# Kernel tuning notes

Hardware: AMD Instinct MI355X
Metric: run time of the kernel (lower is better)

The kernel has to match this reference:

```python
import jax, jax.numpy as jnp
import numpy as np

B, H, S, D = 2, 16, 2048, 64  # batch, heads, seq (q_len=k_len), head dim (d_k=d_v)


def setup_inputs() -> dict:
    key = jax.random.key(0)
    kq, kk, kv = jax.random.split(key, 3)
    Q = jax.random.normal(kq, (B, H, S, D), dtype=jnp.float32)
    K = jax.random.normal(kk, (B, H, S, D), dtype=jnp.float32)
    V = jax.random.normal(kv, (B, H, S, D), dtype=jnp.float32)
    # causal 0/1 mask [q_len, k_len]; zeros get filled with -inf like masked_fill_
    mask = jnp.tril(jnp.ones((S, S), dtype=jnp.int32))
    return {"Q": Q, "K": K, "V": V, "mask": mask}


def reference(Q, K, V, mask):
    scale = K.shape[-1] ** 0.5
    # [B,H,q,k] = Q @ K^T / sqrt(d_k)
    scores = jnp.einsum("bhqd,bhkd->bhqk", Q, K) / scale
    # mask broadcast over batch/heads; mask==0 -> -inf
    scores = jnp.where(mask == 0, jnp.float32(-jnp.inf), scores)
    attn = jax.nn.softmax(scores, axis=-1)
    return jnp.einsum("bhqk,bhkd->bhqd", attn, V)
```

## Files before the change

kernel.cpp:

```cpp
#include <hip/hip_runtime.h>

#define S_LEN 2048
#define DHEAD 64
#define BK 64
#define NBH 32
#define QSCALE 0.18033688011112042f
#define LTHR 1.125899907e15f
#define LSCL 8.881784197e-16f

typedef float f32x4 __attribute__((ext_vector_type(4)));
typedef __bf16 bf16x8 __attribute__((ext_vector_type(8)));
typedef unsigned short u16x8 __attribute__((ext_vector_type(8)));
typedef unsigned short u16x4 __attribute__((ext_vector_type(4)));
typedef unsigned int   u32x4 __attribute__((ext_vector_type(4)));
typedef unsigned int   u32x2 __attribute__((ext_vector_type(2)));

static __device__ __forceinline__ unsigned short bfr(float f) {
    return __builtin_bit_cast(unsigned short, (__bf16)f);
}
static __device__ __forceinline__ int swz(int row, int cb) {
    return row * 128 + (cb ^ ((row & 7) << 4));
}

#if __has_builtin(__builtin_amdgcn_permlane32_swap) && __has_builtin(__builtin_amdgcn_permlane16_swap)
static __device__ __forceinline__ void plswap32(unsigned& a, unsigned& b) {
    u32x2 r = __builtin_amdgcn_permlane32_swap(a, b, false, false);
    a = r[0]; b = r[1];
}
static __device__ __forceinline__ void plswap16(unsigned& a, unsigned& b) {
    u32x2 r = __builtin_amdgcn_permlane16_swap(a, b, false, false);
    a = r[0]; b = r[1];
}
#else
static __device__ __forceinline__ void plswap32(unsigned& a, unsigned& b) {
    asm("v_permlane32_swap_b32 %0, %1" : "+v"(a), "+v"(b));
}
static __device__ __forceinline__ void plswap16(unsigned& a, unsigned& b) {
    asm("v_permlane16_swap_b32 %0, %1" : "+v"(a), "+v"(b));
}
#endif

__global__ __launch_bounds__(256)
void prep(const float* __restrict__ K, const float* __restrict__ V,
          unsigned short* __restrict__ Kb, unsigned short* __restrict__ Vt, int n4) {
    __shared__ unsigned short t2[64][72];
    if ((int)blockIdx.x < 2048) {
        const int stride = 2048 * 256;
        for (int i = (int)blockIdx.x * 256 + threadIdx.x; i < n4; i += stride) {
            f32x4 v = ((const f32x4*)K)[i];
            u16x4 t;
            t[0] = bfr(v[0]); t[1] = bfr(v[1]); t[2] = bfr(v[2]); t[3] = bfr(v[3]);
            ((u16x4*)Kb)[i] = t;
        }
    } else {
        const int bid = (int)blockIdx.x - 2048;
        const int bh = bid >> 5;
        const int st = bid & 31;
        const int t  = threadIdx.x;
        {
            const int sl = t >> 2, d0 = (t & 3) * 16;
            const float* src = V + ((size_t)bh * S_LEN + st * 64 + sl) * DHEAD + d0;
#pragma unroll
            for (int j = 0; j < 4; ++j) {
                f32x4 v = *(const f32x4*)(src + j * 4);
#pragma unroll
                for (int e = 0; e < 4; ++e) t2[sl][d0 + j * 4 + e] = bfr(v[e]);
            }
        }
        __syncthreads();
        const int d = t >> 2, sc = (t & 3) * 16;
        u16x8 a, b;
#pragma unroll
        for (int r = 0; r < 8; ++r) { a[r] = t2[sc + r][d]; b[r] = t2[sc + 8 + r][d]; }
        unsigned short* dst = Vt + ((size_t)bh * DHEAD + d) * S_LEN + st * 64 + sc;
        *(u16x8*)dst = a;
        *(u16x8*)(dst + 8) = b;
    }
}

__global__ __launch_bounds__(256, 3)
void attn_pipe(const float* __restrict__ Qg,
               const unsigned short* __restrict__ Kb,
               const unsigned short* __restrict__ Vt,
               float* __restrict__ Og) {
    __shared__ __align__(16) unsigned short sK[2][BK * DHEAD];
    __shared__ __align__(16) unsigned short sV[2][DHEAD * BK];

    const int tid  = threadIdx.x;
    const int lane = tid & 63;
    const int w    = tid >> 6;
    const int idx = (int)blockIdx.x >> 5;
    const int bh  = (int)blockIdx.x & (NBH - 1);
    const int jj  = idx & 7, k4 = idx >> 3;
    const int blk_q = (k4 == 0) ? 31 - jj : (k4 == 1) ? jj
                    : (k4 == 2) ? 16 + jj : 15 - jj;
    const int q0 = blk_q * 64;
    const size_t base = (size_t)bh * (S_LEN * DHEAD);

    const int c = lane & 15;
    const int h = lane >> 4;

    const int srow = w * 8 + (lane >> 3);
    const int ch8  = ((lane & 7) ^ (lane >> 3)) * 8;
    const unsigned short* pK = Kb + base + (size_t)srow * DHEAD + ch8;
    const unsigned short* pV = Vt + base + (size_t)srow * S_LEN + ch8;

    auto issue = [&](int buf, int kt) {
        unsigned short* dK = &sK[buf][w * 512];
        unsigned short* dV = &sV[buf][w * 512];
        const unsigned short* gk = pK + (size_t)kt * 4096;
        const unsigned short* gv = pV + kt * 64;
#pragma unroll
        for (int i = 0; i < 2; ++i) {
            __builtin_amdgcn_global_load_lds(
                (const __attribute__((address_space(1))) unsigned int*)(gk + i * 2048),
                (__attribute__((address_space(3))) unsigned int*)(dK + i * 2048),
                16, 0, 0);
            __builtin_amdgcn_global_load_lds(
                (const __attribute__((address_space(1))) unsigned int*)(gv + (size_t)i * 32 * S_LEN),
                (__attribute__((address_space(3))) unsigned int*)(dV + i * 2048),
                16, 0, 0);
        }
    };

    bf16x8 qf[2];
    {
        const int qrow = q0 + w * 16 + c;
        const float* qp = Qg + base + (size_t)qrow * DHEAD + h * 8;
#pragma unroll
        for (int kk = 0; kk < 2; ++kk) {
            f32x4 a = *(const f32x4*)(qp + kk * 32);
            f32x4 b = *(const f32x4*)(qp + kk * 32 + 4);
            u16x8 t;
#pragma unroll
            for (int j = 0; j < 4; ++j) {
                t[j]     = bfr(a[j] * QSCALE);
                t[4 + j] = bfr(b[j] * QSCALE);
            }
            qf[kk] = __builtin_bit_cast(bf16x8, t);
        }
    }

    bf16x8 onesf;
    {
        u16x8 t;
#pragma unroll
        for (int j = 0; j < 8; ++j) t[j] = 0x3F80;
        onesf = __builtin_bit_cast(bf16x8, t);
    }

    int offAB[4][2];
#pragma unroll
    for (int n = 0; n < 4; ++n)
#pragma unroll
        for (int kk = 0; kk < 2; ++kk)
            offAB[n][kk] = swz(n * 16 + c, (kk * 32 + h * 8) * 2);

    f32x4 o[4];
#pragma unroll
    for (int dn = 0; dn < 4; ++dn) o[dn] = (f32x4){0.f, 0.f, 0.f, 0.f};
    f32x4 l4 = (f32x4){0.f, 0.f, 0.f, 0.f};
    float m_run = 0.f;
    const int qg = q0 + w * 16 + c;

    issue(0, 0);
    __syncthreads();
    if (blk_q >= 1) issue(1, 1);

    f32x4 st[4];
    {
        const char* sKc = (const char*)&sK[0][0];
#pragma unroll
        for (int n = 0; n < 4; ++n) {
            f32x4 acc = (f32x4){0.f, 0.f, 0.f, 0.f};
#pragma unroll
            for (int kk = 0; kk < 2; ++kk) {
                u16x8 kf = *(const u16x8*)(sKc + offAB[n][kk]);
                acc = __builtin_amdgcn_mfma_f32_16x16x32_bf16(
                        __builtin_bit_cast(bf16x8, kf), qf[kk], acc, 0, 0, 0);
            }
            st[n] = acc;
        }
    }
    bf16x8 vf[4][2];
    {
        const char* sVc = (const char*)&sV[0][0];
#pragma unroll
        for (int dn = 0; dn < 4; ++dn)
#pragma unroll
            for (int kk = 0; kk < 2; ++kk)
                vf[dn][kk] = __builtin_bit_cast(bf16x8,
                                *(const u16x8*)(sVc + offAB[dn][kk]));
    }

    for (int i = 0; i <= blk_q; ++i) {
        f32x4 st2[4];
        bf16x8 vf2[4][2];
        if (i < blk_q) {
            __syncthreads();
            if (i + 2 <= blk_q) issue(i & 1, i + 2);

            const char* sKc = (const char*)&sK[(i + 1) & 1][0];
            const char* sVc = (const char*)&sV[(i + 1) & 1][0];
            const float mb = -m_run;
#pragma unroll
            for (int n = 0; n < 4; ++n) {
                f32x4 acc = (f32x4){mb, mb, mb, mb};
#pragma unroll
                for (int kk = 0; kk < 2; ++kk) {
                    u16x8 kf = *(const u16x8*)(sKc + offAB[n][kk]);
                    acc = __builtin_amdgcn_mfma_f32_16x16x32_bf16(
                            __builtin_bit_cast(bf16x8, kf), qf[kk], acc, 0, 0, 0);
                }
                st2[n] = acc;
            }
#pragma unroll
            for (int dn = 0; dn < 4; ++dn)
#pragma unroll
                for (int kk = 0; kk < 2; ++kk)
                    vf2[dn][kk] = __builtin_bit_cast(bf16x8,
                                    *(const u16x8*)(sVc + offAB[dn][kk]));
        }

        if (i == blk_q) {
#pragma unroll
            for (int n = 0; n < 4; ++n)
#pragma unroll
                for (int r = 0; r < 4; ++r)
                    if (i * BK + n * 16 + 4 * h + r > qg) st[n][r] = -INFINITY;
        }

#pragma unroll
        for (int n = 0; n < 4; ++n)
#pragma unroll
            for (int r = 0; r < 4; ++r)
                st[n][r] = exp2f(st[n][r]);

        unsigned pd[4][2];
#pragma unroll
        for (int n = 0; n < 4; ++n) {
            pd[n][0] = (unsigned)bfr(st[n][0]) | ((unsigned)bfr(st[n][1]) << 16);
            pd[n][1] = (unsigned)bfr(st[n][2]) | ((unsigned)bfr(st[n][3]) << 16);
        }
        bf16x8 pb[2];
#pragma unroll
        for (int kk = 0; kk < 2; ++kk) {
            u32x4 fr;
#pragma unroll
            for (int X = 0; X < 2; ++X) {
                unsigned u = pd[2 * kk][X], v = pd[2 * kk + 1][X];
                plswap32(u, v);
                plswap16(u, v);
                fr[X]     = u;
                fr[2 + X] = v;
            }
            pb[kk] = __builtin_bit_cast(bf16x8, fr);
        }

        __builtin_amdgcn_s_setprio(1);
#pragma unroll
        for (int kk = 0; kk < 2; ++kk) {
            l4 = __builtin_amdgcn_mfma_f32_16x16x32_bf16(onesf, pb[kk], l4, 0, 0, 0);
#pragma unroll
            for (int dn = 0; dn < 4; ++dn)
                o[dn] = __builtin_amdgcn_mfma_f32_16x16x32_bf16(
                          vf[dn][kk], pb[kk], o[dn], 0, 0, 0);
        }
        __builtin_amdgcn_s_setprio(0);

        if (__builtin_expect(l4[0] > LTHR, 0)) {
            m_run += 50.0f;
            l4 *= LSCL;
#pragma unroll
            for (int dn = 0; dn < 4; ++dn) o[dn] *= LSCL;
            if (i < blk_q) {
#pragma unroll
                for (int n = 0; n < 4; ++n)
#pragma unroll
                    for (int r = 0; r < 4; ++r) st2[n][r] -= 50.0f;
            }
        }

        if (i < blk_q) {
#pragma unroll
            for (int n = 0; n < 4; ++n) st[n] = st2[n];
#pragma unroll
            for (int dn = 0; dn < 4; ++dn)
#pragma unroll
                for (int kk = 0; kk < 2; ++kk) vf[dn][kk] = vf2[dn][kk];
        }
    }

    const float inv = 1.0f / l4[0];
    float* op = Og + base + (size_t)qg * DHEAD + h * 4;
#pragma unroll
    for (int dn = 0; dn < 4; ++dn) {
        f32x4 t = o[dn] * inv;
        *(f32x4*)(op + dn * 16) = t;
    }
}

__global__ __launch_bounds__(256)
void attn_fb(const float* __restrict__ Qg, const float* __restrict__ K32,
             const float* __restrict__ V32, float* __restrict__ Og) {
    __shared__ __align__(16) unsigned short sK[2][BK * DHEAD];
    __shared__ __align__(16) unsigned short sV[2][DHEAD * BK];
    __shared__ __align__(16) unsigned short sP[4][16 * BK];

    const int tid  = threadIdx.x;
    const int lane = tid & 63;
    const int w    = tid >> 6;
    const int blk_q = 31 - ((int)blockIdx.x >> 5);
    const int bh    = (int)blockIdx.x & (NBH - 1);
    const int q0    = blk_q * 64;
    const size_t base = (size_t)bh * (S_LEN * DHEAD);

    const int col = lane & 15;
    const int hi  = lane >> 4;
    const int vkb = (tid >> 4) * 4;
    const int vdb = (tid & 15) * 4;
    const int fkr = tid >> 2;
    const int fkc = (tid & 3) * 16;

    f32x4 kr32[4], vr32[4];
    auto stage_issue = [&](int kt) {
        const float* kp = K32 + base + (size_t)(kt * BK + fkr) * DHEAD + fkc;
#pragma unroll
        for (int j = 0; j < 4; ++j) kr32[j] = *(const f32x4*)(kp + j * 4);
        const float* vp = V32 + base + (size_t)(kt * BK + vkb) * DHEAD + vdb;
#pragma unroll
        for (int j = 0; j < 4; ++j) vr32[j] = *(const f32x4*)(vp + j * DHEAD);
    };
    auto stage_write = [&](int buf) {
        char* sKb_ = (char*)&sK[buf][0];
        char* sVb_ = (char*)&sV[buf][0];
        u16x8 p0, p1;
#pragma unroll
        for (int j = 0; j < 4; ++j) {
            p0[j] = bfr(kr32[0][j]); p0[4 + j] = bfr(kr32[1][j]);
            p1[j] = bfr(kr32[2][j]); p1[4 + j] = bfr(kr32[3][j]);
        }
        *(u16x8*)(sKb_ + swz(fkr, fkc * 2))      = p0;
        *(u16x8*)(sKb_ + swz(fkr, fkc * 2 + 16)) = p1;
#pragma unroll
        for (int dd = 0; dd < 4; ++dd) {
            u16x4 t;
#pragma unroll
            for (int j = 0; j < 4; ++j) t[j] = bfr(vr32[j][dd]);
            *(u16x4*)(sVb_ + swz(vdb + dd, vkb * 2)) = t;
        }
    };

    bf16x8 qf[2];
    {
        const int qrow = q0 + w * 16 + col;
        const float* qp = Qg + base + (size_t)qrow * DHEAD + hi * 8;
#pragma unroll
        for (int kk = 0; kk < 2; ++kk) {
            f32x4 a = *(const f32x4*)(qp + kk * 32);
            f32x4 b = *(const f32x4*)(qp + kk * 32 + 4);
            u16x8 t;
#pragma unroll
            for (int j = 0; j < 4; ++j) {
                t[j]     = bfr(a[j] * QSCALE);
                t[4 + j] = bfr(b[j] * QSCALE);
            }
            qf[kk] = __builtin_bit_cast(bf16x8, t);
        }
    }

    int offAB[4][2];
#pragma unroll
    for (int n = 0; n < 4; ++n)
#pragma unroll
        for (int kk = 0; kk < 2; ++kk)
            offAB[n][kk] = swz(n * 16 + col, (kk * 32 + hi * 8) * 2);
    char* sPw = (char*)&sP[w][0];
    int offPS[4], offPL[2];
#pragma unroll
    for (int n = 0; n < 4; ++n)
        offPS[n] = col * 128 + ((n * 32 + hi * 8) ^ ((col & 7) << 4));
#pragma unroll
    for (int kk = 0; kk < 2; ++kk)
        offPL[kk] = col * 128 + ((kk * 64 + hi * 16) ^ ((col & 7) << 4));

    f32x4 o[4];
#pragma unroll
    for (int dn = 0; dn < 4; ++dn) o[dn] = (f32x4){0.f, 0.f, 0.f, 0.f};
    float m_run = -INFINITY, l_run = 0.f;

    stage_issue(0);
    stage_write(0);
    __syncthreads();

    int cur = 0;
    for (int kt = 0; kt <= blk_q; ++kt) {
        const char* sKc = (const char*)&sK[cur][0];
        const char* sVc = (const char*)&sV[cur][0];
        if (kt < blk_q) stage_issue(kt + 1);

        f32x4 st[4];
#pragma unroll
        for (int n = 0; n < 4; ++n) {
            f32x4 acc = (f32x4){0.f, 0.f, 0.f, 0.f};
#pragma unroll
            for (int kk = 0; kk < 2; ++kk) {
                u16x8 kf = *(const u16x8*)(sKc + offAB[n][kk]);
                acc = __builtin_amdgcn_mfma_f32_16x16x32_bf16(
                        __builtin_bit_cast(bf16x8, kf), qf[kk], acc, 0, 0, 0);
            }
            st[n] = acc;
        }
        if (kt == blk_q) {
            const int qg = q0 + w * 16 + col;
#pragma unroll
            for (int n = 0; n < 4; ++n)
#pragma unroll
                for (int r = 0; r < 4; ++r)
                    if (kt * BK + n * 16 + hi * 4 + r > qg) st[n][r] = -INFINITY;
        }
        float mx = fmaxf(fmaxf(st[0][0], st[0][1]), fmaxf(st[0][2], st[0][3]));
#pragma unroll
        for (int n = 1; n < 4; ++n)
            mx = fmaxf(mx, fmaxf(fmaxf(st[n][0], st[n][1]), fmaxf(st[n][2], st[n][3])));
        mx = fmaxf(mx, __shfl_xor(mx, 16));
        mx = fmaxf(mx, __shfl_xor(mx, 32));
        if (!__all(mx <= m_run + 8.0f)) {
            const float mn = fmaxf(m_run, mx);
            const float al = exp2f(m_run - mn);
            m_run = mn;
            l_run *= al;
#pragma unroll
            for (int dn = 0; dn < 4; ++dn) o[dn] *= al;
        }
        float sum = 0.f;
#pragma unroll
        for (int n = 0; n < 4; ++n)
#pragma unroll
            for (int r = 0; r < 4; ++r) {
                float p = exp2f(st[n][r] - m_run);
                st[n][r] = p;
                sum += p;
            }
        sum += __shfl_xor(sum, 16);
        sum += __shfl_xor(sum, 32);
        l_run += sum;
#pragma unroll
        for (int n = 0; n < 4; ++n) {
            u16x4 t;
#pragma unroll
            for (int r = 0; r < 4; ++r) t[r] = bfr(st[n][r]);
            *(u16x4*)(sPw + offPS[n]) = t;
        }
        bf16x8 pb[2];
#pragma unroll
        for (int kk = 0; kk < 2; ++kk)
            pb[kk] = __builtin_bit_cast(bf16x8, *(const u16x8*)(sPw + offPL[kk]));
#pragma unroll
        for (int dn = 0; dn < 4; ++dn)
#pragma unroll
            for (int kk = 0; kk < 2; ++kk) {
                u16x8 vfr = *(const u16x8*)(sVc + offAB[dn][kk]);
                o[dn] = __builtin_amdgcn_mfma_f32_16x16x32_bf16(
                          __builtin_bit_cast(bf16x8, vfr), pb[kk], o[dn], 0, 0, 0);
            }
        if (kt < blk_q) stage_write(cur ^ 1);
        __syncthreads();
        cur ^= 1;
    }

    const float inv = 1.0f / l_run;
    const int qg = q0 + w * 16 + col;
    float* op = Og + base + (size_t)qg * DHEAD + hi * 4;
#pragma unroll
    for (int dn = 0; dn < 4; ++dn) {
        f32x4 t = o[dn] * inv;
        *(f32x4*)(op + dn * 16) = t;
    }
}

extern "C" void kernel_launch(void* const* d_in, const int* in_sizes, int n_in,
                              void* d_out, int out_size, void* d_ws, size_t ws_size,
                              hipStream_t stream) {
    const float* Q = (const float*)d_in[0];
    const float* K = (const float*)d_in[1];
    const float* V = (const float*)d_in[2];
    float* O = (float*)d_out;

    const size_t nelem   = (size_t)NBH * S_LEN * DHEAD;
    const size_t kvBytes = 2 * nelem * sizeof(unsigned short);

    if (ws_size >= kvBytes) {
        unsigned short* Kb = (unsigned short*)d_ws;
        unsigned short* Vt = Kb + nelem;
        prep<<<3072, 256, 0, stream>>>(K, V, Kb, Vt, (int)(nelem / 4));
        attn_pipe<<<dim3(32 * NBH), 256, 0, stream>>>(Q, Kb, Vt, O);
    } else {
        attn_fb<<<dim3(32 * NBH), 256, 0, stream>>>(Q, K, V, O);
    }
}
```

Before: 55.77 us.

## Process 128-row query tiles with two 16-row subtiles per wave

```diff
diff --git a/kernel.cpp b/kernel.cpp
--- a/kernel.cpp
+++ b/kernel.cpp
@@ -78,27 +78,27 @@
     }
 }
 
-__global__ __launch_bounds__(256, 3)
-void attn_pipe(const float* __restrict__ Qg,
-               const unsigned short* __restrict__ Kb,
-               const unsigned short* __restrict__ Vt,
-               float* __restrict__ Og) {
+__global__ __launch_bounds__(256, 2)
+void attn2q(const float* __restrict__ Qg,
+            const unsigned short* __restrict__ Kb,
+            const unsigned short* __restrict__ Vt,
+            float* __restrict__ Og) {
     __shared__ __align__(16) unsigned short sK[2][BK * DHEAD];
     __shared__ __align__(16) unsigned short sV[2][DHEAD * BK];
 
     const int tid  = threadIdx.x;
     const int lane = tid & 63;
     const int w    = tid >> 6;
-    const int idx = (int)blockIdx.x >> 5;
-    const int bh  = (int)blockIdx.x & (NBH - 1);
-    const int jj  = idx & 7, k4 = idx >> 3;
-    const int blk_q = (k4 == 0) ? 31 - jj : (k4 == 1) ? jj
-                    : (k4 == 2) ? 16 + jj : 15 - jj;
-    const int q0 = blk_q * 64;
+    const int bh = (int)blockIdx.x & (NBH - 1);
+    const int j  = (int)blockIdx.x >> 5;
+    const int qb = (j < 8) ? 15 - j : j - 8;
+    const int q0 = qb * 128;
+    const int ktmax = 2 * qb + 1;
     const size_t base = (size_t)bh * (S_LEN * DHEAD);
 
     const int c = lane & 15;
     const int h = lane >> 4;
+    const int qrow0 = q0 + w * 32;
 
     const int srow = w * 8 + (lane >> 3);
     const int ch8  = ((lane & 7) ^ (lane >> 3)) * 8;
@@ -123,9 +123,10 @@
         }
     };
 
-    bf16x8 qf[2];
-    {
-        const int qrow = q0 + w * 16 + c;
+    bf16x8 qf[2][2];
+#pragma unroll
+    for (int qt = 0; qt < 2; ++qt) {
+        const int qrow = qrow0 + qt * 16 + c;
         const float* qp = Qg + base + (size_t)qrow * DHEAD + h * 8;
 #pragma unroll
         for (int kk = 0; kk < 2; ++kk) {
@@ -133,11 +134,11 @@
             f32x4 b = *(const f32x4*)(qp + kk * 32 + 4);
             u16x8 t;
 #pragma unroll
-            for (int j = 0; j < 4; ++j) {
-                t[j]     = bfr(a[j] * QSCALE);
-                t[4 + j] = bfr(b[j] * QSCALE);
-            }
-            qf[kk] = __builtin_bit_cast(bf16x8, t);
+            for (int jj = 0; jj < 4; ++jj) {
+                t[jj]     = bfr(a[jj] * QSCALE);
+                t[4 + jj] = bfr(b[jj] * QSCALE);
+            }
+            qf[qt][kk] = __builtin_bit_cast(bf16x8, t);
         }
     }
 
@@ -145,7 +146,7 @@
     {
         u16x8 t;
 #pragma unroll
-        for (int j = 0; j < 8; ++j) t[j] = 0x3F80;
+        for (int jj = 0; jj < 8; ++jj) t[jj] = 0x3F80;
         onesf = __builtin_bit_cast(bf16x8, t);
     }
 
@@ -156,147 +157,143 @@
         for (int kk = 0; kk < 2; ++kk)
             offAB[n][kk] = swz(n * 16 + c, (kk * 32 + h * 8) * 2);
 
-    f32x4 o[4];
-#pragma unroll
-    for (int dn = 0; dn < 4; ++dn) o[dn] = (f32x4){0.f, 0.f, 0.f, 0.f};
-    f32x4 l4 = (f32x4){0.f, 0.f, 0.f, 0.f};
-    float m_run = 0.f;
-    const int qg = q0 + w * 16 + c;
+    f32x4 o[2][4];
+#pragma unroll
+    for (int qt = 0; qt < 2; ++qt)
+#pragma unroll
+        for (int dn = 0; dn < 4; ++dn) o[qt][dn] = (f32x4){0.f, 0.f, 0.f, 0.f};
+    f32x4 l4[2];
+    l4[0] = (f32x4){0.f, 0.f, 0.f, 0.f};
+    l4[1] = (f32x4){0.f, 0.f, 0.f, 0.f};
+    float m_run[2] = {0.f, 0.f};
 
     issue(0, 0);
-    __syncthreads();
-    if (blk_q >= 1) issue(1, 1);
-
-    f32x4 st[4];
-    {
-        const char* sKc = (const char*)&sK[0][0];
-#pragma unroll
-        for (int n = 0; n < 4; ++n) {
-            f32x4 acc = (f32x4){0.f, 0.f, 0.f, 0.f};
-#pragma unroll
-            for (int kk = 0; kk < 2; ++kk) {
-                u16x8 kf = *(const u16x8*)(sKc + offAB[n][kk]);
-                acc = __builtin_amdgcn_mfma_f32_16x16x32_bf16(
-                        __builtin_bit_cast(bf16x8, kf), qf[kk], acc, 0, 0, 0);
-            }
-            st[n] = acc;
-        }
-    }
-    bf16x8 vf[4][2];
-    {
-        const char* sVc = (const char*)&sV[0][0];
-#pragma unroll
-        for (int dn = 0; dn < 4; ++dn)
-#pragma unroll
-            for (int kk = 0; kk < 2; ++kk)
-                vf[dn][kk] = __builtin_bit_cast(bf16x8,
-                                *(const u16x8*)(sVc + offAB[dn][kk]));
-    }
-
-    for (int i = 0; i <= blk_q; ++i) {
-        f32x4 st2[4];
-        bf16x8 vf2[4][2];
-        if (i < blk_q) {
-            __syncthreads();
-            if (i + 2 <= blk_q) issue(i & 1, i + 2);
-
-            const char* sKc = (const char*)&sK[(i + 1) & 1][0];
-            const char* sVc = (const char*)&sV[(i + 1) & 1][0];
-            const float mb = -m_run;
-#pragma unroll
-            for (int n = 0; n < 4; ++n) {
-                f32x4 acc = (f32x4){mb, mb, mb, mb};
+    int cur = 0;
+    for (int kt = 0; kt <= ktmax; ++kt) {
+        __syncthreads();
+        if (kt < ktmax) issue(cur ^ 1, kt + 1);
+
+        if ((kt << 6) <= qrow0 + 31) {
+            const char* sKc = (const char*)&sK[cur][0];
+            const char* sVc = (const char*)&sV[cur][0];
+
+            bf16x8 kr[4][2];
+#pragma unroll
+            for (int n = 0; n < 4; ++n)
+#pragma unroll
+                for (int kk = 0; kk < 2; ++kk)
+                    kr[n][kk] = __builtin_bit_cast(bf16x8,
+                                    *(const u16x8*)(sKc + offAB[n][kk]));
+
+            f32x4 st[2][4];
+            __builtin_amdgcn_s_setprio(1);
+#pragma unroll
+            for (int qt = 0; qt < 2; ++qt) {
+                const float mb = -m_run[qt];
+#pragma unroll
+                for (int n = 0; n < 4; ++n) {
+                    f32x4 acc = (f32x4){mb, mb, mb, mb};
+#pragma unroll
+                    for (int kk = 0; kk < 2; ++kk)
+                        acc = __builtin_amdgcn_mfma_f32_16x16x32_bf16(
+                                kr[n][kk], qf[qt][kk], acc, 0, 0, 0);
+                    st[qt][n] = acc;
+                }
+            }
+            __builtin_amdgcn_s_setprio(0);
+
+            bf16x8 vf[4][2];
+#pragma unroll
+            for (int dn = 0; dn < 4; ++dn)
+#pragma unroll
+                for (int kk = 0; kk < 2; ++kk)
+                    vf[dn][kk] = __builtin_bit_cast(bf16x8,
+                                    *(const u16x8*)(sVc + offAB[dn][kk]));
+
+            if ((kt << 6) + 63 > qrow0) {
+#pragma unroll
+                for (int qt = 0; qt < 2; ++qt) {
+                    const int qg = qrow0 + qt * 16 + c;
+#pragma unroll
+                    for (int n = 0; n < 4; ++n)
+#pragma unroll
+                        for (int r = 0; r < 4; ++r)
+                            if ((kt << 6) + n * 16 + 4 * h + r > qg)
+                                st[qt][n][r] = -INFINITY;
+                }
+            }
+
+#pragma unroll
+            for (int qt = 0; qt < 2; ++qt)
+#pragma unroll
+                for (int n = 0; n < 4; ++n)
+#pragma unroll
+                    for (int r = 0; r < 4; ++r)
+                        st[qt][n][r] = exp2f(st[qt][n][r]);
+
+            bf16x8 pb[2][2];
+#pragma unroll
+            for (int qt = 0; qt < 2; ++qt) {
+                unsigned pd[4][2];
+#pragma unroll
+                for (int n = 0; n < 4; ++n) {
+                    pd[n][0] = (unsigned)bfr(st[qt][n][0]) |
+                               ((unsigned)bfr(st[qt][n][1]) << 16);
+                    pd[n][1] = (unsigned)bfr(st[qt][n][2]) |
+                               ((unsigned)bfr(st[qt][n][3]) << 16);
+                }
 #pragma unroll
                 for (int kk = 0; kk < 2; ++kk) {
-                    u16x8 kf = *(const u16x8*)(sKc + offAB[n][kk]);
-                    acc = __builtin_amdgcn_mfma_f32_16x16x32_bf16(
-                            __builtin_bit_cast(bf16x8, kf), qf[kk], acc, 0, 0, 0);
-                }
-                st2[n] = acc;
-            }
-#pragma unroll
-            for (int dn = 0; dn < 4; ++dn)
-#pragma unroll
-                for (int kk = 0; kk < 2; ++kk)
-                    vf2[dn][kk] = __builtin_bit_cast(bf16x8,
-                                    *(const u16x8*)(sVc + offAB[dn][kk]));
-        }
-
-        if (i == blk_q) {
-#pragma unroll
-            for (int n = 0; n < 4; ++n)
-#pragma unroll
-                for (int r = 0; r < 4; ++r)
-                    if (i * BK + n * 16 + 4 * h + r > qg) st[n][r] = -INFINITY;
-        }
-
-#pragma unroll
-        for (int n = 0; n < 4; ++n)
-#pragma unroll
-            for (int r = 0; r < 4; ++r)
-                st[n][r] = exp2f(st[n][r]);
-
-        unsigned pd[4][2];
-#pragma unroll
-        for (int n = 0; n < 4; ++n) {
-            pd[n][0] = (unsigned)bfr(st[n][0]) | ((unsigned)bfr(st[n][1]) << 16);
-            pd[n][1] = (unsigned)bfr(st[n][2]) | ((unsigned)bfr(st[n][3]) << 16);
-        }
-        bf16x8 pb[2];
-#pragma unroll
-        for (int kk = 0; kk < 2; ++kk) {
-            u32x4 fr;
-#pragma unroll
-            for (int X = 0; X < 2; ++X) {
-                unsigned u = pd[2 * kk][X], v = pd[2 * kk + 1][X];
-                plswap32(u, v);
-                plswap16(u, v);
-                fr[X]     = u;
-                fr[2 + X] = v;
-            }
-            pb[kk] = __builtin_bit_cast(bf16x8, fr);
-        }
-
-        __builtin_amdgcn_s_setprio(1);
-#pragma unroll
-        for (int kk = 0; kk < 2; ++kk) {
-            l4 = __builtin_amdgcn_mfma_f32_16x16x32_bf16(onesf, pb[kk], l4, 0, 0, 0);
-#pragma unroll
-            for (int dn = 0; dn < 4; ++dn)
-                o[dn] = __builtin_amdgcn_mfma_f32_16x16x32_bf16(
-                          vf[dn][kk], pb[kk], o[dn], 0, 0, 0);
-        }
-        __builtin_amdgcn_s_setprio(0);
-
-        if (__builtin_expect(l4[0] > LTHR, 0)) {
-            m_run += 50.0f;
-            l4 *= LSCL;
-#pragma unroll
-            for (int dn = 0; dn < 4; ++dn) o[dn] *= LSCL;
-            if (i < blk_q) {
-#pragma unroll
-                for (int n = 0; n < 4; ++n)
-#pragma unroll
-                    for (int r = 0; r < 4; ++r) st2[n][r] -= 50.0f;
-            }
-        }
-
-        if (i < blk_q) {
-#pragma unroll
-            for (int n = 0; n < 4; ++n) st[n] = st2[n];
-#pragma unroll
-            for (int dn = 0; dn < 4; ++dn)
-#pragma unroll
-                for (int kk = 0; kk < 2; ++kk) vf[dn][kk] = vf2[dn][kk];
-        }
-    }
-
-    const float inv = 1.0f / l4[0];
-    float* op = Og + base + (size_t)qg * DHEAD + h * 4;
-#pragma unroll
-    for (int dn = 0; dn < 4; ++dn) {
-        f32x4 t = o[dn] * inv;
-        *(f32x4*)(op + dn * 16) = t;
+                    u32x4 fr;
+#pragma unroll
+                    for (int X = 0; X < 2; ++X) {
+                        unsigned u = pd[2 * kk][X], v = pd[2 * kk + 1][X];
+                        plswap32(u, v);
+                        plswap16(u, v);
+                        fr[X]     = u;
+                        fr[2 + X] = v;
+                    }
+                    pb[qt][kk] = __builtin_bit_cast(bf16x8, fr);
+                }
+            }
+
+            __builtin_amdgcn_s_setprio(1);
+#pragma unroll
+            for (int qt = 0; qt < 2; ++qt)
+#pragma unroll
+                for (int kk = 0; kk < 2; ++kk) {
+                    l4[qt] = __builtin_amdgcn_mfma_f32_16x16x32_bf16(
+                               onesf, pb[qt][kk], l4[qt], 0, 0, 0);
+#pragma unroll
+                    for (int dn = 0; dn < 4; ++dn)
+                        o[qt][dn] = __builtin_amdgcn_mfma_f32_16x16x32_bf16(
+                                      vf[dn][kk], pb[qt][kk], o[qt][dn], 0, 0, 0);
+                }
+            __builtin_amdgcn_s_setprio(0);
+
+#pragma unroll
+            for (int qt = 0; qt < 2; ++qt) {
+                if (__builtin_expect(l4[qt][0] > LTHR, 0)) {
+                    m_run[qt] += 50.0f;
+                    l4[qt] *= LSCL;
+#pragma unroll
+                    for (int dn = 0; dn < 4; ++dn) o[qt][dn] *= LSCL;
+                }
+            }
+        }
+        cur ^= 1;
+    }
+
+#pragma unroll
+    for (int qt = 0; qt < 2; ++qt) {
+        const float inv = 1.0f / l4[qt][0];
+        const int qg = qrow0 + qt * 16 + c;
+        float* op = Og + base + (size_t)qg * DHEAD + h * 4;
+#pragma unroll
+        for (int dn = 0; dn < 4; ++dn) {
+            f32x4 t = o[qt][dn] * inv;
+            *(f32x4*)(op + dn * 16) = t;
+        }
     }
 }
 
@@ -494,7 +491,7 @@
         unsigned short* Kb = (unsigned short*)d_ws;
         unsigned short* Vt = Kb + nelem;
         prep<<<3072, 256, 0, stream>>>(K, V, Kb, Vt, (int)(nelem / 4));
-        attn_pipe<<<dim3(32 * NBH), 256, 0, stream>>>(Q, Kb, Vt, O);
+        attn2q<<<dim3(16 * NBH), 256, 0, stream>>>(Q, Kb, Vt, O);
     } else {
         attn_fb<<<dim3(32 * NBH), 256, 0, stream>>>(Q, K, V, O);
     }
```

Result: slower. 65.37 us (+17.2%).
